# Optimization experiments

Measured on AMD Instinct MI355X. Metric: run time of the kernel, lower is better.

Reference implementation:

```python
import jax, jax.numpy as jnp
import numpy as np

H = 16            # L-BFGS history length
N = 4_000_000     # number of parameters
HIGH = jax.lax.Precision.HIGHEST


def setup_inputs() -> dict:
    key = jax.random.key(0)
    k1, k2, k3 = jax.random.split(key, 3)
    # Small-scale steps so inner products are well conditioned.
    y = jax.random.normal(k1, (H, N), jnp.float32) * 0.01           # S_k: parameter diffs
    g = y + 0.1 * jax.random.normal(k2, (H, N), jnp.float32) * 0.01  # Y_k: grad diffs, s_i.g_i > 0
    pytree = jax.random.normal(k3, (N,), jnp.float32)
    sy = jnp.dot(y, g.T, precision=HIGH)                 # [H,H] s_i . y_j
    cross = jnp.tril(sy, k=-1)                           # L_k (strictly lower triangular)
    diag = jnp.diag(sy)                                  # diag(D_k), positive by construction
    s_inner = jnp.dot(y, y.T, precision=HIGH)            # S^T S
    return {
        "pytree": pytree,
        "y_diff_history": y,
        "grad_diff_history": g,
        "y_diff_grad_diff_cross_inner": cross,
        "y_diff_grad_diff_inner": diag,
        "y_diff_cross_inner": s_inner,
        "index_start": 21,  # > H: buffer full, circular-roll branch active
    }


def reference(pytree, y_diff_history, grad_diff_history,
              y_diff_grad_diff_cross_inner, y_diff_grad_diff_inner,
              y_diff_cross_inner, index_start):
    h = y_diff_history.shape[0]
    idx = (index_start - 1) % h
    s_last = y_diff_history[idx]
    g_last = grad_diff_history[idx]
    curvature = jnp.dot(s_last, g_last, precision=HIGH)
    gamma = jnp.where(curvature > 0,
                      jnp.dot(g_last, g_last, precision=HIGH) / curvature,
                      jnp.float32(1.0))
    d = jnp.where(y_diff_grad_diff_inner == 0, 1.0, y_diff_grad_diff_inner)
    L = y_diff_grad_diff_cross_inner
    # J J^T = gamma * S^T S + L D^-1 L^T
    J_square = gamma * y_diff_cross_inner + jnp.dot(L / d, L.T, precision=HIGH)
    J = jnp.linalg.cholesky(J_square)
    # Project input onto the two history bases: [2H]
    top = jnp.einsum('hn,n->h', grad_diff_history, pytree, precision=HIGH)
    bot = gamma * jnp.einsum('hn,n->h', y_diff_history, pytree, precision=HIGH)
    descent = jnp.concatenate([top, bot])
    roll_by = -(index_start % h)

    def maybe_roll(v, r):
        return jax.lax.cond(index_start <= h, lambda x: x, lambda x: jnp.roll(x, r), v)

    descent = descent.at[:h].set(maybe_roll(descent[:h], roll_by))
    descent = descent.at[h:].set(maybe_roll(descent[h:], roll_by))
    sqrt_d = jnp.sqrt(d)
    low_tri = jnp.block([
        [jnp.diag(sqrt_d), jnp.zeros((h, h), descent.dtype)],
        [-L / sqrt_d, J],
    ])
    descent = jax.scipy.linalg.solve_triangular(low_tri, descent, lower=True)
    upper_tri = low_tri.T
    upper_tri = upper_tri.at[:h].set(-upper_tri[:h])
    descent = jax.scipy.linalg.solve_triangular(upper_tri, descent, lower=False)
    descent = descent.at[:h].set(maybe_roll(descent[:h], -roll_by))
    descent = descent.at[h:].set(maybe_roll(descent[h:], -roll_by))
    out = (gamma * pytree
           - jnp.einsum('h,hn->n', descent[:h], grad_diff_history, precision=HIGH)
           - gamma * jnp.einsum('h,hn->n', descent[h:], y_diff_history, precision=HIGH))
    return out
```

## Files before the change

### kernel.cpp

```cpp
#include <hip/hip_runtime.h>

#define HH 16
#define RED_VALS 34

__global__ __launch_bounds__(256) void lbfgs_reduce(
    const float* __restrict__ p, const float* __restrict__ y,
    const float* __restrict__ g, const int* __restrict__ idxp,
    float* __restrict__ partials, int n) {
  const int is = idxp[0];
  const int hidx = ((is - 1) % HH + HH) % HH;
  float acc[RED_VALS];
#pragma unroll
  for (int j = 0; j < RED_VALS; ++j) acc[j] = 0.f;

  const int tid = blockIdx.x * blockDim.x + threadIdx.x;
  const int nth = gridDim.x * blockDim.x;
  const int nchunk = n >> 2;
  const float4* __restrict__ p4 = reinterpret_cast<const float4*>(p);

  for (int c = tid; c < nchunk; c += nth) {
    float4 pv = p4[c];
#pragma unroll
    for (int i = 0; i < HH; ++i) {
      const float4 gv = reinterpret_cast<const float4*>(g + (size_t)i * n)[c];
      const float4 yv = reinterpret_cast<const float4*>(y + (size_t)i * n)[c];
      acc[i]      += gv.x * pv.x + gv.y * pv.y + gv.z * pv.z + gv.w * pv.w;
      acc[HH + i] += yv.x * pv.x + yv.y * pv.y + yv.z * pv.z + yv.w * pv.w;
      if (i == hidx) {
        acc[32] += yv.x * gv.x + yv.y * gv.y + yv.z * gv.z + yv.w * gv.w;
        acc[33] += gv.x * gv.x + gv.y * gv.y + gv.z * gv.z + gv.w * gv.w;
      }
    }
  }
  for (int c = (nchunk << 2) + tid; c < n; c += nth) {
    float pv = p[c];
#pragma unroll
    for (int i = 0; i < HH; ++i) {
      float gv = g[(size_t)i * n + c];
      float yv = y[(size_t)i * n + c];
      acc[i] += gv * pv;
      acc[HH + i] += yv * pv;
      if (i == hidx) { acc[32] += yv * gv; acc[33] += gv * gv; }
    }
  }
#pragma unroll
  for (int j = 0; j < RED_VALS; ++j) {
    float v = acc[j];
#pragma unroll
    for (int off = 32; off > 0; off >>= 1) v += __shfl_down(v, off);
    acc[j] = v;
  }
  __shared__ float red[4][RED_VALS];
  const int wave = threadIdx.x >> 6, lane = threadIdx.x & 63;
  if (lane == 0) {
#pragma unroll
    for (int j = 0; j < RED_VALS; ++j) red[wave][j] = acc[j];
  }
  __syncthreads();
  if (threadIdx.x < RED_VALS) {
    float s = red[0][threadIdx.x] + red[1][threadIdx.x] +
              red[2][threadIdx.x] + red[3][threadIdx.x];
    partials[(size_t)blockIdx.x * RED_VALS + threadIdx.x] = s;
  }
}

__global__ __launch_bounds__(256) void lbfgs_solve(
    const float* __restrict__ partials, int nblk,
    const float* __restrict__ Lmat, const float* __restrict__ diag,
    const float* __restrict__ sinner, const int* __restrict__ idxp,
    float* __restrict__ coeff) {
  __shared__ float sums[RED_VALS];
  __shared__ float wred[RED_VALS][4];
  const int wave = threadIdx.x >> 6, lane = threadIdx.x & 63;
  for (int j = 0; j < RED_VALS; ++j) {
    float v = 0.f;
    for (int b = threadIdx.x; b < nblk; b += 256)
      v += partials[(size_t)b * RED_VALS + j];
#pragma unroll
    for (int off = 32; off > 0; off >>= 1) v += __shfl_down(v, off);
    if (lane == 0) wred[j][wave] = v;
  }
  __syncthreads();
  if (threadIdx.x < RED_VALS)
    sums[threadIdx.x] = wred[threadIdx.x][0] + wred[threadIdx.x][1] +
                        wred[threadIdx.x][2] + wred[threadIdx.x][3];
  __syncthreads();

  __shared__ float Lsh[HH][HH];
  __shared__ float dd[HH], sqd[HH];
  __shared__ float Jsq[HH][HH];
  __shared__ float gamma_s;
  __shared__ float x[2 * HH];
  {
    int i = threadIdx.x >> 4, j = threadIdx.x & 15;
    if (threadIdx.x < 256) Lsh[i][j] = Lmat[i * HH + j];
  }
  if (threadIdx.x < HH) {
    float dv = diag[threadIdx.x];
    float ddv = (dv == 0.f) ? 1.f : dv;
    dd[threadIdx.x] = ddv;
    sqd[threadIdx.x] = sqrtf(ddv);
  }
  if (threadIdx.x == 0) {
    float cur = sums[32], gg = sums[33];
    gamma_s = (cur > 0.f) ? (gg / cur) : 1.f;
  }
  __syncthreads();
  {
    int i = threadIdx.x >> 4, j = threadIdx.x & 15;
    float v = gamma_s * sinner[i * HH + j];
#pragma unroll
    for (int k = 0; k < HH; ++k) v += Lsh[i][k] * Lsh[j][k] / dd[k];
    Jsq[i][j] = v;
  }
  __syncthreads();
  if (threadIdx.x == 0) {
    for (int c = 0; c < HH; ++c) {
      float s = Jsq[c][c];
      for (int k = 0; k < c; ++k) s -= Jsq[c][k] * Jsq[c][k];
      float dv = sqrtf(s);
      Jsq[c][c] = dv;
      float inv = 1.f / dv;
      for (int r = c + 1; r < HH; ++r) {
        float s2 = Jsq[r][c];
        for (int k = 0; k < c; ++k) s2 -= Jsq[r][k] * Jsq[c][k];
        Jsq[r][c] = s2 * inv;
      }
    }
    const int is = idxp[0];
    const int sh = (is <= HH) ? 0 : (is % HH);
    const float gamma = gamma_s;
    for (int k = 0; k < HH; ++k) {
      x[k]      = sums[(k + sh) & (HH - 1)];
      x[HH + k] = gamma * sums[HH + ((k + sh) & (HH - 1))];
    }
    for (int i = 0; i < HH; ++i) x[i] /= sqd[i];
    for (int i = 0; i < HH; ++i) {
      float s = x[HH + i];
      for (int j = 0; j < HH; ++j) s += (Lsh[i][j] / sqd[j]) * x[j];
      for (int j = 0; j < i; ++j) s -= Jsq[i][j] * x[HH + j];
      x[HH + i] = s / Jsq[i][i];
    }
    for (int i = HH - 1; i >= 0; --i) {
      float s = x[HH + i];
      for (int j = i + 1; j < HH; ++j) s -= Jsq[j][i] * x[HH + j];
      x[HH + i] = s / Jsq[i][i];
    }
    for (int i = 0; i < HH; ++i) {
      float s = x[i];
      for (int j = 0; j < HH; ++j) s -= (Lsh[j][i] / sqd[i]) * x[HH + j];
      x[i] = s / (-sqd[i]);
    }
    coeff[0] = gamma;
    for (int k = 0; k < HH; ++k) {
      coeff[1 + k]      = x[(k - sh + HH) & (HH - 1)];
      coeff[1 + HH + k] = gamma * x[HH + ((k - sh + HH) & (HH - 1))];
    }
  }
}

__global__ __launch_bounds__(256) void lbfgs_output(
    const float* __restrict__ p, const float* __restrict__ y,
    const float* __restrict__ g, const float* __restrict__ coeff,
    float* __restrict__ out, int n) {
  const float gamma = coeff[0];
  float a[HH], b[HH];
#pragma unroll
  for (int i = 0; i < HH; ++i) {
    a[i] = coeff[1 + i];
    b[i] = coeff[1 + HH + i];
  }
  const int tid = blockIdx.x * blockDim.x + threadIdx.x;
  const int nth = gridDim.x * blockDim.x;
  const int nchunk = n >> 2;
  const float4* __restrict__ p4 = reinterpret_cast<const float4*>(p);
  float4* __restrict__ out4 = reinterpret_cast<float4*>(out);
  for (int c = tid; c < nchunk; c += nth) {
    float4 pv = p4[c];
    float ox = gamma * pv.x, oy = gamma * pv.y;
    float oz = gamma * pv.z, ow = gamma * pv.w;
#pragma unroll
    for (int i = 0; i < HH; ++i) {
      const float4 gv = reinterpret_cast<const float4*>(g + (size_t)i * n)[c];
      const float4 yv = reinterpret_cast<const float4*>(y + (size_t)i * n)[c];
      ox -= a[i] * gv.x + b[i] * yv.x;
      oy -= a[i] * gv.y + b[i] * yv.y;
      oz -= a[i] * gv.z + b[i] * yv.z;
      ow -= a[i] * gv.w + b[i] * yv.w;
    }
    out4[c] = make_float4(ox, oy, oz, ow);
  }
  for (int c = (nchunk << 2) + tid; c < n; c += nth) {
    float pv = p[c];
    float o = gamma * pv;
#pragma unroll
    for (int i = 0; i < HH; ++i)
      o -= a[i] * g[(size_t)i * n + c] + b[i] * y[(size_t)i * n + c];
    out[c] = o;
  }
}

extern "C" void kernel_launch(void* const* d_in, const int* in_sizes, int n_in,
                              void* d_out, int out_size, void* d_ws, size_t ws_size,
                              hipStream_t stream) {
  const float* p      = (const float*)d_in[0];
  const float* y      = (const float*)d_in[1];
  const float* g      = (const float*)d_in[2];
  const float* Lmat   = (const float*)d_in[3];
  const float* diag   = (const float*)d_in[4];
  const float* sinner = (const float*)d_in[5];
  const int*   idxp   = (const int*)d_in[6];
  float* out = (float*)d_out;
  float* wsf = (float*)d_ws;
  const int n = in_sizes[0];

  int nblk = 1024;
  size_t need = (size_t)(nblk * RED_VALS + 64) * sizeof(float);
  if (ws_size < need) {
    long avail = (long)(ws_size / sizeof(float)) - 64;
    nblk = (int)(avail / RED_VALS);
    if (nblk < 1) nblk = 1;
    if (nblk > 1024) nblk = 1024;
  }
  float* partials = wsf;
  float* coeff = wsf + (size_t)nblk * RED_VALS;

  lbfgs_reduce<<<dim3(nblk), dim3(256), 0, stream>>>(p, y, g, idxp, partials, n);
  lbfgs_solve<<<dim3(1), dim3(256), 0, stream>>>(partials, nblk, Lmat, diag,
                                                 sinner, idxp, coeff);
  lbfgs_output<<<dim3(nblk), dim3(256), 0, stream>>>(p, y, g, coeff, out, n);
}
```

Measured before the change: 258.4 us.

## Split reduction across history rows with 2D grid, enlarge output grid

The projection kernel now uses a 2D grid with one row of blocks per history index, so each thread keeps 4 accumulators instead of 34 and streams only one g/y row plus p. This cuts register pressure and raises occupancy, at the cost of rereading p from memory 16 times. The solve kernel reindexes the new partials layout, and the output kernel launches 2048 blocks instead of 1024.

```diff
diff --git a/kernel.cpp b/kernel.cpp
--- a/kernel.cpp
+++ b/kernel.cpp
@@ -1,81 +1,85 @@
 #include <hip/hip_runtime.h>
 
 #define HH 16
+#define GX 256
 #define RED_VALS 34
 
 __global__ __launch_bounds__(256) void lbfgs_reduce(
     const float* __restrict__ p, const float* __restrict__ y,
     const float* __restrict__ g, const int* __restrict__ idxp,
     float* __restrict__ partials, int n) {
+  const int row = blockIdx.y;
   const int is = idxp[0];
   const int hidx = ((is - 1) % HH + HH) % HH;
-  float acc[RED_VALS];
-#pragma unroll
-  for (int j = 0; j < RED_VALS; ++j) acc[j] = 0.f;
-
+  const bool special = (row == hidx);
+
+  const float4* __restrict__ p4 = reinterpret_cast<const float4*>(p);
+  const float4* __restrict__ g4 = reinterpret_cast<const float4*>(g + (size_t)row * n);
+  const float4* __restrict__ y4 = reinterpret_cast<const float4*>(y + (size_t)row * n);
+
+  float ag = 0.f, ay = 0.f, ac = 0.f, agg = 0.f;
   const int tid = blockIdx.x * blockDim.x + threadIdx.x;
   const int nth = gridDim.x * blockDim.x;
   const int nchunk = n >> 2;
-  const float4* __restrict__ p4 = reinterpret_cast<const float4*>(p);
 
   for (int c = tid; c < nchunk; c += nth) {
     float4 pv = p4[c];
-#pragma unroll
-    for (int i = 0; i < HH; ++i) {
-      const float4 gv = reinterpret_cast<const float4*>(g + (size_t)i * n)[c];
-      const float4 yv = reinterpret_cast<const float4*>(y + (size_t)i * n)[c];
-      acc[i]      += gv.x * pv.x + gv.y * pv.y + gv.z * pv.z + gv.w * pv.w;
-      acc[HH + i] += yv.x * pv.x + yv.y * pv.y + yv.z * pv.z + yv.w * pv.w;
-      if (i == hidx) {
-        acc[32] += yv.x * gv.x + yv.y * gv.y + yv.z * gv.z + yv.w * gv.w;
-        acc[33] += gv.x * gv.x + gv.y * gv.y + gv.z * gv.z + gv.w * gv.w;
-      }
+    float4 gv = g4[c];
+    float4 yv = y4[c];
+    ag += gv.x * pv.x + gv.y * pv.y + gv.z * pv.z + gv.w * pv.w;
+    ay += yv.x * pv.x + yv.y * pv.y + yv.z * pv.z + yv.w * pv.w;
+    if (special) {
+      ac  += yv.x * gv.x + yv.y * gv.y + yv.z * gv.z + yv.w * gv.w;
+      agg += gv.x * gv.x + gv.y * gv.y + gv.z * gv.z + gv.w * gv.w;
     }
   }
   for (int c = (nchunk << 2) + tid; c < n; c += nth) {
     float pv = p[c];
-#pragma unroll
-    for (int i = 0; i < HH; ++i) {
-      float gv = g[(size_t)i * n + c];
-      float yv = y[(size_t)i * n + c];
-      acc[i] += gv * pv;
-      acc[HH + i] += yv * pv;
-      if (i == hidx) { acc[32] += yv * gv; acc[33] += gv * gv; }
-    }
-  }
-#pragma unroll
-  for (int j = 0; j < RED_VALS; ++j) {
-    float v = acc[j];
+    float gv = g[(size_t)row * n + c];
+    float yv = y[(size_t)row * n + c];
+    ag += gv * pv;
+    ay += yv * pv;
+    if (special) { ac += yv * gv; agg += gv * gv; }
+  }
+
+  float vals[4] = {ag, ay, ac, agg};
+#pragma unroll
+  for (int j = 0; j < 4; ++j) {
+    float v = vals[j];
 #pragma unroll
     for (int off = 32; off > 0; off >>= 1) v += __shfl_down(v, off);
-    acc[j] = v;
-  }
-  __shared__ float red[4][RED_VALS];
+    vals[j] = v;
+  }
+  __shared__ float red[4][4];
   const int wave = threadIdx.x >> 6, lane = threadIdx.x & 63;
   if (lane == 0) {
 #pragma unroll
-    for (int j = 0; j < RED_VALS; ++j) red[wave][j] = acc[j];
-  }
-  __syncthreads();
-  if (threadIdx.x < RED_VALS) {
+    for (int j = 0; j < 4; ++j) red[wave][j] = vals[j];
+  }
+  __syncthreads();
+  if (threadIdx.x < 4) {
     float s = red[0][threadIdx.x] + red[1][threadIdx.x] +
               red[2][threadIdx.x] + red[3][threadIdx.x];
-    partials[(size_t)blockIdx.x * RED_VALS + threadIdx.x] = s;
+    partials[((size_t)row * gridDim.x + blockIdx.x) * 4 + threadIdx.x] = s;
   }
 }
 
 __global__ __launch_bounds__(256) void lbfgs_solve(
-    const float* __restrict__ partials, int nblk,
+    const float* __restrict__ partials, int nblkx,
     const float* __restrict__ Lmat, const float* __restrict__ diag,
     const float* __restrict__ sinner, const int* __restrict__ idxp,
     float* __restrict__ coeff) {
+  const int is = idxp[0];
+  const int hidx = ((is - 1) % HH + HH) % HH;
   __shared__ float sums[RED_VALS];
   __shared__ float wred[RED_VALS][4];
   const int wave = threadIdx.x >> 6, lane = threadIdx.x & 63;
   for (int j = 0; j < RED_VALS; ++j) {
+    const int row  = (j < HH) ? j : (j < 2 * HH ? j - HH : hidx);
+    const int comp = (j < HH) ? 0 : (j < 2 * HH ? 1 : (j == 32 ? 2 : 3));
     float v = 0.f;
-    for (int b = threadIdx.x; b < nblk; b += 256)
-      v += partials[(size_t)b * RED_VALS + j];
+    for (int b = threadIdx.x; b < nblkx; b += 256)
+      v += partials[((size_t)row * nblkx + b) * 4 + comp];
 #pragma unroll
     for (int off = 32; off > 0; off >>= 1) v += __shfl_down(v, off);
     if (lane == 0) wred[j][wave] = v;
@@ -127,7 +131,6 @@
         Jsq[r][c] = s2 * inv;
       }
     }
-    const int is = idxp[0];
     const int sh = (is <= HH) ? 0 : (is % HH);
     const float gamma = gamma_s;
     for (int k = 0; k < HH; ++k) {
@@ -214,19 +217,19 @@
   float* wsf = (float*)d_ws;
   const int n = in_sizes[0];
 
-  int nblk = 1024;
-  size_t need = (size_t)(nblk * RED_VALS + 64) * sizeof(float);
+  int gx = GX;
+  size_t need = ((size_t)HH * gx * 4 + 64) * sizeof(float);
   if (ws_size < need) {
     long avail = (long)(ws_size / sizeof(float)) - 64;
-    nblk = (int)(avail / RED_VALS);
-    if (nblk < 1) nblk = 1;
-    if (nblk > 1024) nblk = 1024;
+    gx = (int)(avail / (HH * 4));
+    if (gx < 1) gx = 1;
+    if (gx > GX) gx = GX;
   }
   float* partials = wsf;
-  float* coeff = wsf + (size_t)nblk * RED_VALS;
-
-  lbfgs_reduce<<<dim3(nblk), dim3(256), 0, stream>>>(p, y, g, idxp, partials, n);
-  lbfgs_solve<<<dim3(1), dim3(256), 0, stream>>>(partials, nblk, Lmat, diag,
+  float* coeff = wsf + (size_t)HH * gx * 4;
+
+  lbfgs_reduce<<<dim3(gx, HH), dim3(256), 0, stream>>>(p, y, g, idxp, partials, n);
+  lbfgs_solve<<<dim3(1), dim3(256), 0, stream>>>(partials, gx, Lmat, diag,
                                                  sinner, idxp, coeff);
-  lbfgs_output<<<dim3(nblk), dim3(256), 0, stream>>>(p, y, g, coeff, out, n);
-}
+  lbfgs_output<<<dim3(2048), dim3(256), 0, stream>>>(p, y, g, coeff, out, n);
+}
```

Result: faster. 236.5 us (-8.5%).

## Reverse output sweep to reuse cache, hoist curvature row, double grid

Applied to the files above, without the earlier changes.

The output kernel now walks its grid-stride chunks in reverse order, so the tail of y/g last read by the reduce kernel, which may still be in the large last-level cache, is consumed first. The curvature and gradient-norm dot products use dedicated loads of the last history row instead of a branch inside the unrolled loop. The grid grows to 2048 blocks, and the output kernel always launches 2048 even when the workspace caps the reduce grid. These changes trade an extra row read per chunk, which should hit cache, for less branching and more reuse of cached data across the two passes.

```diff
diff --git a/kernel.cpp b/kernel.cpp
--- a/kernel.cpp
+++ b/kernel.cpp
@@ -2,6 +2,7 @@
 
 #define HH 16
 #define RED_VALS 34
+#define NBLK 2048
 
 __global__ __launch_bounds__(256) void lbfgs_reduce(
     const float* __restrict__ p, const float* __restrict__ y,
@@ -9,6 +10,7 @@
     float* __restrict__ partials, int n) {
   const int is = idxp[0];
   const int hidx = ((is - 1) % HH + HH) % HH;
+
   float acc[RED_VALS];
 #pragma unroll
   for (int j = 0; j < RED_VALS; ++j) acc[j] = 0.f;
@@ -16,31 +18,34 @@
   const int tid = blockIdx.x * blockDim.x + threadIdx.x;
   const int nth = gridDim.x * blockDim.x;
   const int nchunk = n >> 2;
-  const float4* __restrict__ p4 = reinterpret_cast<const float4*>(p);
+  const float4* __restrict__ p4  = reinterpret_cast<const float4*>(p);
+  const float4* __restrict__ gh4 = reinterpret_cast<const float4*>(g + (size_t)hidx * n);
+  const float4* __restrict__ yh4 = reinterpret_cast<const float4*>(y + (size_t)hidx * n);
 
   for (int c = tid; c < nchunk; c += nth) {
-    float4 pv = p4[c];
+    float4 pv  = p4[c];
+    float4 ghv = gh4[c];
+    float4 yhv = yh4[c];
+    acc[32] += yhv.x * ghv.x + yhv.y * ghv.y + yhv.z * ghv.z + yhv.w * ghv.w;
+    acc[33] += ghv.x * ghv.x + ghv.y * ghv.y + ghv.z * ghv.z + ghv.w * ghv.w;
 #pragma unroll
     for (int i = 0; i < HH; ++i) {
       const float4 gv = reinterpret_cast<const float4*>(g + (size_t)i * n)[c];
       const float4 yv = reinterpret_cast<const float4*>(y + (size_t)i * n)[c];
       acc[i]      += gv.x * pv.x + gv.y * pv.y + gv.z * pv.z + gv.w * pv.w;
       acc[HH + i] += yv.x * pv.x + yv.y * pv.y + yv.z * pv.z + yv.w * pv.w;
-      if (i == hidx) {
-        acc[32] += yv.x * gv.x + yv.y * gv.y + yv.z * gv.z + yv.w * gv.w;
-        acc[33] += gv.x * gv.x + gv.y * gv.y + gv.z * gv.z + gv.w * gv.w;
-      }
     }
   }
   for (int c = (nchunk << 2) + tid; c < n; c += nth) {
     float pv = p[c];
-#pragma unroll
-    for (int i = 0; i < HH; ++i) {
-      float gv = g[(size_t)i * n + c];
-      float yv = y[(size_t)i * n + c];
-      acc[i] += gv * pv;
-      acc[HH + i] += yv * pv;
-      if (i == hidx) { acc[32] += yv * gv; acc[33] += gv * gv; }
+    float ghv = g[(size_t)hidx * n + c];
+    float yhv = y[(size_t)hidx * n + c];
+    acc[32] += yhv * ghv;
+    acc[33] += ghv * ghv;
+#pragma unroll
+    for (int i = 0; i < HH; ++i) {
+      acc[i]      += g[(size_t)i * n + c] * pv;
+      acc[HH + i] += y[(size_t)i * n + c] * pv;
     }
   }
 #pragma unroll
@@ -175,7 +180,19 @@
   const int nchunk = n >> 2;
   const float4* __restrict__ p4 = reinterpret_cast<const float4*>(p);
   float4* __restrict__ out4 = reinterpret_cast<float4*>(out);
-  for (int c = tid; c < nchunk; c += nth) {
+
+  for (int c = (nchunk << 2) + tid; c < n; c += nth) {
+    float pv = p[c];
+    float o = gamma * pv;
+#pragma unroll
+    for (int i = 0; i < HH; ++i)
+      o -= a[i] * g[(size_t)i * n + c] + b[i] * y[(size_t)i * n + c];
+    out[c] = o;
+  }
+  const int nsteps = (nchunk + nth - 1) / nth;
+  for (int s = nsteps - 1; s >= 0; --s) {
+    const int c = tid + s * nth;
+    if (c >= nchunk) continue;
     float4 pv = p4[c];
     float ox = gamma * pv.x, oy = gamma * pv.y;
     float oz = gamma * pv.z, ow = gamma * pv.w;
@@ -189,14 +206,6 @@
       ow -= a[i] * gv.w + b[i] * yv.w;
     }
     out4[c] = make_float4(ox, oy, oz, ow);
-  }
-  for (int c = (nchunk << 2) + tid; c < n; c += nth) {
-    float pv = p[c];
-    float o = gamma * pv;
-#pragma unroll
-    for (int i = 0; i < HH; ++i)
-      o -= a[i] * g[(size_t)i * n + c] + b[i] * y[(size_t)i * n + c];
-    out[c] = o;
   }
 }
 
@@ -214,13 +223,13 @@
   float* wsf = (float*)d_ws;
   const int n = in_sizes[0];
 
-  int nblk = 1024;
-  size_t need = (size_t)(nblk * RED_VALS + 64) * sizeof(float);
+  int nblk = NBLK;
+  size_t need = ((size_t)nblk * RED_VALS + 64) * sizeof(float);
   if (ws_size < need) {
     long avail = (long)(ws_size / sizeof(float)) - 64;
     nblk = (int)(avail / RED_VALS);
     if (nblk < 1) nblk = 1;
-    if (nblk > 1024) nblk = 1024;
+    if (nblk > NBLK) nblk = NBLK;
   }
   float* partials = wsf;
   float* coeff = wsf + (size_t)nblk * RED_VALS;
@@ -228,5 +237,5 @@
   lbfgs_reduce<<<dim3(nblk), dim3(256), 0, stream>>>(p, y, g, idxp, partials, n);
   lbfgs_solve<<<dim3(1), dim3(256), 0, stream>>>(partials, nblk, Lmat, diag,
                                                  sinner, idxp, coeff);
-  lbfgs_output<<<dim3(nblk), dim3(256), 0, stream>>>(p, y, g, coeff, out, n);
-}
+  lbfgs_output<<<dim3(NBLK), dim3(256), 0, stream>>>(p, y, g, coeff, out, n);
+}
```

Result: slower. 294.3 us (+13.9%).

## Split reduction across history groups in a 2D grid and enlarge output grid

Applied to the files above, without the earlier changes.

The reduction kernel now uses a 2D grid. Four y-groups each handle four history rows, and a fifth group computes the curvature and gradient-norm dot products from the last history row only. This cuts per-thread accumulators from 34 to 8 and removes the per-row branch, with the aim of raising occupancy and memory-level parallelism. The cost is that p is re-read four times and the last history row is read again. The output kernel's block count is also doubled, and the solve kernel's partial indexing is remapped to the new layout.

```diff
diff --git a/kernel.cpp b/kernel.cpp
--- a/kernel.cpp
+++ b/kernel.cpp
@@ -2,70 +2,93 @@
 
 #define HH 16
 #define RED_VALS 34
+#define RGX 1024
+#define OUTBLK 2048
 
 __global__ __launch_bounds__(256) void lbfgs_reduce(
     const float* __restrict__ p, const float* __restrict__ y,
     const float* __restrict__ g, const int* __restrict__ idxp,
     float* __restrict__ partials, int n) {
-  const int is = idxp[0];
-  const int hidx = ((is - 1) % HH + HH) % HH;
-  float acc[RED_VALS];
-#pragma unroll
-  for (int j = 0; j < RED_VALS; ++j) acc[j] = 0.f;
-
+  const int grp = blockIdx.y;
   const int tid = blockIdx.x * blockDim.x + threadIdx.x;
   const int nth = gridDim.x * blockDim.x;
   const int nchunk = n >> 2;
-  const float4* __restrict__ p4 = reinterpret_cast<const float4*>(p);
-
-  for (int c = tid; c < nchunk; c += nth) {
-    float4 pv = p4[c];
-#pragma unroll
-    for (int i = 0; i < HH; ++i) {
-      const float4 gv = reinterpret_cast<const float4*>(g + (size_t)i * n)[c];
-      const float4 yv = reinterpret_cast<const float4*>(y + (size_t)i * n)[c];
-      acc[i]      += gv.x * pv.x + gv.y * pv.y + gv.z * pv.z + gv.w * pv.w;
-      acc[HH + i] += yv.x * pv.x + yv.y * pv.y + yv.z * pv.z + yv.w * pv.w;
-      if (i == hidx) {
-        acc[32] += yv.x * gv.x + yv.y * gv.y + yv.z * gv.z + yv.w * gv.w;
-        acc[33] += gv.x * gv.x + gv.y * gv.y + gv.z * gv.z + gv.w * gv.w;
+
+  float acc[8];
+#pragma unroll
+  for (int j = 0; j < 8; ++j) acc[j] = 0.f;
+
+  if (grp < 4) {
+    const float4* __restrict__ p4 = reinterpret_cast<const float4*>(p);
+    const float4* __restrict__ g0 = reinterpret_cast<const float4*>(g + (size_t)(4 * grp + 0) * n);
+    const float4* __restrict__ g1 = reinterpret_cast<const float4*>(g + (size_t)(4 * grp + 1) * n);
+    const float4* __restrict__ g2 = reinterpret_cast<const float4*>(g + (size_t)(4 * grp + 2) * n);
+    const float4* __restrict__ g3 = reinterpret_cast<const float4*>(g + (size_t)(4 * grp + 3) * n);
+    const float4* __restrict__ y0 = reinterpret_cast<const float4*>(y + (size_t)(4 * grp + 0) * n);
+    const float4* __restrict__ y1 = reinterpret_cast<const float4*>(y + (size_t)(4 * grp + 1) * n);
+    const float4* __restrict__ y2 = reinterpret_cast<const float4*>(y + (size_t)(4 * grp + 2) * n);
+    const float4* __restrict__ y3 = reinterpret_cast<const float4*>(y + (size_t)(4 * grp + 3) * n);
+    for (int c = tid; c < nchunk; c += nth) {
+      float4 pv = p4[c];
+      float4 gv0 = g0[c], gv1 = g1[c], gv2 = g2[c], gv3 = g3[c];
+      float4 yv0 = y0[c], yv1 = y1[c], yv2 = y2[c], yv3 = y3[c];
+      acc[0] += gv0.x * pv.x + gv0.y * pv.y + gv0.z * pv.z + gv0.w * pv.w;
+      acc[1] += gv1.x * pv.x + gv1.y * pv.y + gv1.z * pv.z + gv1.w * pv.w;
+      acc[2] += gv2.x * pv.x + gv2.y * pv.y + gv2.z * pv.z + gv2.w * pv.w;
+      acc[3] += gv3.x * pv.x + gv3.y * pv.y + gv3.z * pv.z + gv3.w * pv.w;
+      acc[4] += yv0.x * pv.x + yv0.y * pv.y + yv0.z * pv.z + yv0.w * pv.w;
+      acc[5] += yv1.x * pv.x + yv1.y * pv.y + yv1.z * pv.z + yv1.w * pv.w;
+      acc[6] += yv2.x * pv.x + yv2.y * pv.y + yv2.z * pv.z + yv2.w * pv.w;
+      acc[7] += yv3.x * pv.x + yv3.y * pv.y + yv3.z * pv.z + yv3.w * pv.w;
+    }
+    for (int c = (nchunk << 2) + tid; c < n; c += nth) {
+      float pv = p[c];
+#pragma unroll
+      for (int i = 0; i < 4; ++i) {
+        acc[i]     += g[(size_t)(4 * grp + i) * n + c] * pv;
+        acc[4 + i] += y[(size_t)(4 * grp + i) * n + c] * pv;
       }
     }
-  }
-  for (int c = (nchunk << 2) + tid; c < n; c += nth) {
-    float pv = p[c];
-#pragma unroll
-    for (int i = 0; i < HH; ++i) {
-      float gv = g[(size_t)i * n + c];
-      float yv = y[(size_t)i * n + c];
-      acc[i] += gv * pv;
-      acc[HH + i] += yv * pv;
-      if (i == hidx) { acc[32] += yv * gv; acc[33] += gv * gv; }
-    }
-  }
-#pragma unroll
-  for (int j = 0; j < RED_VALS; ++j) {
+  } else {
+    const int is = idxp[0];
+    const int hidx = ((is - 1) % HH + HH) % HH;
+    const float4* __restrict__ gh4 = reinterpret_cast<const float4*>(g + (size_t)hidx * n);
+    const float4* __restrict__ yh4 = reinterpret_cast<const float4*>(y + (size_t)hidx * n);
+    for (int c = tid; c < nchunk; c += nth) {
+      float4 gv = gh4[c], yv = yh4[c];
+      acc[0] += yv.x * gv.x + yv.y * gv.y + yv.z * gv.z + yv.w * gv.w;
+      acc[1] += gv.x * gv.x + gv.y * gv.y + gv.z * gv.z + gv.w * gv.w;
+    }
+    for (int c = (nchunk << 2) + tid; c < n; c += nth) {
+      float gv = g[(size_t)hidx * n + c], yv = y[(size_t)hidx * n + c];
+      acc[0] += yv * gv;
+      acc[1] += gv * gv;
+    }
+  }
+
+#pragma unroll
+  for (int j = 0; j < 8; ++j) {
     float v = acc[j];
 #pragma unroll
     for (int off = 32; off > 0; off >>= 1) v += __shfl_down(v, off);
     acc[j] = v;
   }
-  __shared__ float red[4][RED_VALS];
+  __shared__ float red[4][8];
   const int wave = threadIdx.x >> 6, lane = threadIdx.x & 63;
   if (lane == 0) {
 #pragma unroll
-    for (int j = 0; j < RED_VALS; ++j) red[wave][j] = acc[j];
-  }
-  __syncthreads();
-  if (threadIdx.x < RED_VALS) {
+    for (int j = 0; j < 8; ++j) red[wave][j] = acc[j];
+  }
+  __syncthreads();
+  if (threadIdx.x < 8) {
     float s = red[0][threadIdx.x] + red[1][threadIdx.x] +
               red[2][threadIdx.x] + red[3][threadIdx.x];
-    partials[(size_t)blockIdx.x * RED_VALS + threadIdx.x] = s;
+    partials[((size_t)grp * gridDim.x + blockIdx.x) * 8 + threadIdx.x] = s;
   }
 }
 
 __global__ __launch_bounds__(256) void lbfgs_solve(
-    const float* __restrict__ partials, int nblk,
+    const float* __restrict__ partials, int nblkx,
     const float* __restrict__ Lmat, const float* __restrict__ diag,
     const float* __restrict__ sinner, const int* __restrict__ idxp,
     float* __restrict__ coeff) {
@@ -73,9 +96,13 @@
   __shared__ float wred[RED_VALS][4];
   const int wave = threadIdx.x >> 6, lane = threadIdx.x & 63;
   for (int j = 0; j < RED_VALS; ++j) {
+    int grpi, slot;
+    if (j < HH)           { grpi = j >> 2;         slot = j & 3; }
+    else if (j < 2 * HH)  { int r = j - HH; grpi = r >> 2; slot = 4 + (r & 3); }
+    else                  { grpi = 4;              slot = j - 32; }
     float v = 0.f;
-    for (int b = threadIdx.x; b < nblk; b += 256)
-      v += partials[(size_t)b * RED_VALS + j];
+    for (int b = threadIdx.x; b < nblkx; b += 256)
+      v += partials[((size_t)grpi * nblkx + b) * 8 + slot];
 #pragma unroll
     for (int off = 32; off > 0; off >>= 1) v += __shfl_down(v, off);
     if (lane == 0) wred[j][wave] = v;
@@ -214,19 +241,19 @@
   float* wsf = (float*)d_ws;
   const int n = in_sizes[0];
 
-  int nblk = 1024;
-  size_t need = (size_t)(nblk * RED_VALS + 64) * sizeof(float);
+  int gx = RGX;
+  size_t need = ((size_t)5 * gx * 8 + 64) * sizeof(float);
   if (ws_size < need) {
     long avail = (long)(ws_size / sizeof(float)) - 64;
-    nblk = (int)(avail / RED_VALS);
-    if (nblk < 1) nblk = 1;
-    if (nblk > 1024) nblk = 1024;
+    gx = (int)(avail / (5 * 8));
+    if (gx < 1) gx = 1;
+    if (gx > RGX) gx = RGX;
   }
   float* partials = wsf;
-  float* coeff = wsf + (size_t)nblk * RED_VALS;
-
-  lbfgs_reduce<<<dim3(nblk), dim3(256), 0, stream>>>(p, y, g, idxp, partials, n);
-  lbfgs_solve<<<dim3(1), dim3(256), 0, stream>>>(partials, nblk, Lmat, diag,
+  float* coeff = wsf + (size_t)5 * gx * 8;
+
+  lbfgs_reduce<<<dim3(gx, 5), dim3(256), 0, stream>>>(p, y, g, idxp, partials, n);
+  lbfgs_solve<<<dim3(1), dim3(256), 0, stream>>>(partials, gx, Lmat, diag,
                                                  sinner, idxp, coeff);
-  lbfgs_output<<<dim3(nblk), dim3(256), 0, stream>>>(p, y, g, coeff, out, n);
-}
+  lbfgs_output<<<dim3(OUTBLK), dim3(256), 0, stream>>>(p, y, g, coeff, out, n);
+}
```

Result: no change. 253.4 us (-1.9%).
